# Optimization experiments

Hardware: AMD Instinct MI355X
Metric: run time of the kernel (lower is better)

## Reference

```python
import jax, jax.numpy as jnp
import numpy as np

N, K, D = 65536, 1024, 512


def setup_inputs() -> dict:
    key = jax.random.key(0)
    k1, k2, k3 = jax.random.split(key, 3)
    x = jax.random.normal(k1, (N, D), dtype=jnp.float32)
    y = jax.random.randint(k2, (N,), 0, K)  # true/assigned cluster labels
    centers = jax.random.normal(k3, (K, D), dtype=jnp.float32)  # nn.Parameter
    return {"x": x, "y": y, "centers": centers}


def reference(x, y, centers):
    # caldis: squared euclidean distance from every point to every center.
    # original expand+sub+square+sum without materializing [N, K, D]).
    x2 = jnp.sum(x * x, axis=1, keepdims=True)          # [N, 1]
    c2 = jnp.sum(centers * centers, axis=1)              # [K]
    distance = x2 - 2.0 * (x @ centers.T) + c2           # [N, K]

    # predict: torch.sort(distance)[1][:, 0] == index of the smallest distance
    ynew = jnp.argmin(distance, axis=1)                  # [N]

    # calwei + calloss: one-hot(y) * distance summed == gather distance[i, y[i]]
    loss = jnp.sum(jnp.take_along_axis(distance, y[:, None], axis=1))

    return loss, ynew
```

## Files before the change

### kernel.cpp

```cpp
#include <hip/hip_runtime.h>

#define NPTS 65536
#define KC   1024
#define DD   512

using bf16x8 = __attribute__((ext_vector_type(8))) __bf16;
using f32x4  = __attribute__((ext_vector_type(4))) float;

__device__ __forceinline__ void gld_lds16(const void* g, void* lds_base) {
  __builtin_amdgcn_global_load_lds(
      (const __attribute__((address_space(1))) unsigned int*)(uintptr_t)g,
      (__attribute__((address_space(3))) unsigned int*)(unsigned int)(uintptr_t)lds_base,
      16, 0, 0);
}

__device__ __forceinline__ uint2 pack4(const float4& v) {
  uint2 r;
  r.x = (__float_as_uint(v.x) >> 16) | (__float_as_uint(v.y) & 0xffff0000u);
  r.y = (__float_as_uint(v.z) >> 16) | (__float_as_uint(v.w) & 0xffff0000u);
  return r;
}


__global__ __launch_bounds__(256) void convert_x_loss(
    const float* __restrict__ x, const int* __restrict__ y,
    const float* __restrict__ centers, uint4* __restrict__ xb,
    float* __restrict__ partial) {
  const int w = threadIdx.x >> 6, l = threadIdx.x & 63;
  const int row = blockIdx.x * 4 + w;
  const float4* xr = (const float4*)(x + (size_t)row * DD);
  float4 a = xr[2 * l];
  float4 b = xr[2 * l + 1];
  uint2 pa = pack4(a), pb = pack4(b);
  xb[row * 64 + l] = make_uint4(pa.x, pa.y, pb.x, pb.y);
  const int yr = y[row];
  const float4* cr = (const float4*)(centers + (size_t)yr * DD);
  float4 ca = cr[2 * l];
  float4 cb = cr[2 * l + 1];
  float d0 = a.x - ca.x, d1 = a.y - ca.y, d2 = a.z - ca.z, d3 = a.w - ca.w;
  float d4 = b.x - cb.x, d5 = b.y - cb.y, d6 = b.z - cb.z, d7 = b.w - cb.w;
  float s = d0 * d0 + d1 * d1 + d2 * d2 + d3 * d3 +
            d4 * d4 + d5 * d5 + d6 * d6 + d7 * d7;
#pragma unroll
  for (int off = 32; off; off >>= 1) s += __shfl_down(s, off, 64);
  __shared__ float ps[4];
  if (l == 0) ps[w] = s;
  __syncthreads();
  if (threadIdx.x == 0) partial[blockIdx.x] = ps[0] + ps[1] + ps[2] + ps[3];
}

__global__ __launch_bounds__(256) void convert_c(
    const float* __restrict__ centers, uint4* __restrict__ cb,
    float* __restrict__ c2) {
  const int row = (blockIdx.x * 256 + threadIdx.x) >> 6;
  const int l = threadIdx.x & 63;
  const float4* cf4 = (const float4*)centers;
  float4 a = cf4[row * 128 + 2 * l];
  float4 b = cf4[row * 128 + 2 * l + 1];
  uint2 pa = pack4(a), pb = pack4(b);
  cb[row * 64 + l] = make_uint4(pa.x, pa.y, pb.x, pb.y);
  float s = a.x * a.x + a.y * a.y + a.z * a.z + a.w * a.w +
            b.x * b.x + b.y * b.y + b.z * b.z + b.w * b.w;
#pragma unroll
  for (int off = 32; off; off >>= 1) s += __shfl_down(s, off, 64);
  if (l == 0) c2[row] = s;
}

__global__ __launch_bounds__(256, 2) void gemm_argmin(
    const uint4* __restrict__ xb, const uint4* __restrict__ cb,
    const float* __restrict__ c2, float* __restrict__ ynew_out) {
  __shared__ uint4 As[1024];
  __shared__ uint4 Bs[2048];
  __shared__ float c2s[1024];

  const int t = threadIdx.x;
  const int w = t >> 6, l = t & 63;
  const int wm = w >> 1, wn = w & 1;
  const int q4 = l >> 4, m16 = l & 15;
  const int row0 = blockIdx.x * 128;

#pragma unroll
  for (int i = 0; i < 4; i++) c2s[t + 256 * i] = c2[t + 256 * i];

  const int r_l = l >> 3;
  const int o_l = (l & 7) ^ r_l;
  int aidx[4];
#pragma unroll
  for (int q = 0; q < 4; q++)
    aidx[q] = (row0 + (w * 4 + q) * 8 + r_l) * 64 + o_l;
  int bsrc[8];
#pragma unroll
  for (int q = 0; q < 8; q++)
    bsrc[q] = ((w * 8 + q) * 8 + r_l) * 64 + o_l;

  const int xr = m16 & 7;

  float best[16];
  int bi_[16];
#pragma unroll
  for (int i = 0; i < 16; i++) { best[i] = 3.4e38f; bi_[i] = 0; }

  for (int n0 = 0; n0 < KC; n0 += 256) {
    f32x4 acc[4][8];
#pragma unroll
    for (int i = 0; i < 4; i++)
#pragma unroll
      for (int j = 0; j < 8; j++) acc[i][j] = (f32x4){0.f, 0.f, 0.f, 0.f};

    const uint4* bbase = cb + n0 * 64;

    for (int ks = 0; ks < 8; ks++) {
      __syncthreads();
#pragma unroll
      for (int q = 0; q < 4; q++)
        gld_lds16(xb + aidx[q] + ks * 8, &As[(w * 4 + q) * 64]);
#pragma unroll
      for (int q = 0; q < 8; q++)
        gld_lds16(bbase + bsrc[q] + ks * 8, &Bs[(w * 8 + q) * 64]);
      __syncthreads();
#pragma unroll
      for (int kk = 0; kk < 2; kk++) {
        const int oct = kk * 4 + q4;
        bf16x8 af[4];
#pragma unroll
        for (int i = 0; i < 4; i++) {
          const int ra = wm * 64 + i * 16 + m16;
          af[i] = *(const bf16x8*)&As[ra * 8 + (oct ^ xr)];
        }
#pragma unroll
        for (int j = 0; j < 8; j++) {
          const int rb = wn * 128 + j * 16 + m16;
          bf16x8 bf = *(const bf16x8*)&Bs[rb * 8 + (oct ^ xr)];
#pragma unroll
          for (int i = 0; i < 4; i++)
            acc[i][j] = __builtin_amdgcn_mfma_f32_16x16x32_bf16(af[i], bf, acc[i][j], 0, 0, 0);
        }
      }
    }

#pragma unroll
    for (int j = 0; j < 8; j++) {
      const int n = n0 + wn * 128 + j * 16 + m16;
      const float cc = c2s[n];
#pragma unroll
      for (int i = 0; i < 4; i++)
#pragma unroll
        for (int r = 0; r < 4; r++) {
          float v = fmaf(-2.f, acc[i][j][r], cc);
          const int bi = i * 4 + r;
          if (v < best[bi]) { best[bi] = v; bi_[bi] = n; }
        }
    }
  }

#pragma unroll
  for (int bi = 0; bi < 16; bi++) {
    float v = best[bi];
    int idx = bi_[bi];
#pragma unroll
    for (int off = 8; off; off >>= 1) {
      float ov = __shfl_xor(v, off, 64);
      int oi = __shfl_xor(idx, off, 64);
      if (ov < v || (ov == v && oi < idx)) { v = ov; idx = oi; }
    }
    if (m16 == 0) {
      const int m = wm * 64 + (bi >> 2) * 16 + q4 * 4 + (bi & 3);
      ynew_out[row0 + m] = (float)idx;
    }
  }
}

__global__ __launch_bounds__(256) void loss_final(const float* __restrict__ partial,
                                                  float* __restrict__ out) {
  float s = 0.f;
#pragma unroll
  for (int j = 0; j < 64; j++) s += partial[threadIdx.x + 256 * j];
#pragma unroll
  for (int off = 32; off; off >>= 1) s += __shfl_down(s, off, 64);
  __shared__ float ps[4];
  if ((threadIdx.x & 63) == 0) ps[threadIdx.x >> 6] = s;
  __syncthreads();
  if (threadIdx.x == 0) out[0] = ps[0] + ps[1] + ps[2] + ps[3];
}


#define SLOT(row, oct) (16 * (oct) + (((row) & 15) ^ (((oct) & 2) << 1)))

__device__ __forceinline__ void split_pack(const float4& a, const float4& b,
                                           uint4& hi, uint4& lo) {
  float f[8] = {a.x, a.y, a.z, a.w, b.x, b.y, b.z, b.w};
  uint hw[4], lw[4];
#pragma unroll
  for (int i = 0; i < 4; i++) {
    uint e0 = __float_as_uint(f[2 * i]), e1 = __float_as_uint(f[2 * i + 1]);
    hw[i] = (e0 >> 16) | (e1 & 0xffff0000u);
    float l0 = f[2 * i]     - __uint_as_float(e0 & 0xffff0000u);
    float l1 = f[2 * i + 1] - __uint_as_float(e1 & 0xffff0000u);
    lw[i] = (__float_as_uint(l0) >> 16) | (__float_as_uint(l1) & 0xffff0000u);
  }
  hi = make_uint4(hw[0], hw[1], hw[2], hw[3]);
  lo = make_uint4(lw[0], lw[1], lw[2], lw[3]);
}

__global__ __launch_bounds__(256) void c2_kernel(const float* __restrict__ centers,
                                                 float* __restrict__ c2) {
  int wave = (blockIdx.x * 256 + threadIdx.x) >> 6;
  int lane = threadIdx.x & 63;
  const float4* c4 = (const float4*)(centers + (size_t)wave * DD);
  float s = 0.f;
#pragma unroll
  for (int j = 0; j < 2; j++) {
    float4 v = c4[lane + 64 * j];
    s += v.x * v.x + v.y * v.y + v.z * v.z + v.w * v.w;
  }
#pragma unroll
  for (int off = 32; off; off >>= 1) s += __shfl_down(s, off, 64);
  if (lane == 0) c2[wave] = s;
}

__global__ __launch_bounds__(256, 2) void argmin_fb(
    const float* __restrict__ x, const float* __restrict__ centers,
    const float* __restrict__ c2, float* __restrict__ ynew_out) {
  __shared__ uint4 Ah[512], Al[512], Bh[512], Bl[512];
  const int t = threadIdx.x;
  const int w = t >> 6, l = t & 63;
  const int wm = w >> 1, wn = w & 1;
  const size_t row0 = (size_t)blockIdx.x * 128;
  const int srow = t >> 1, h = t & 1;
  const int mt = srow >> 4;
  const int so0 = mt * 64 + SLOT(srow, 2 * h);
  const int so1 = mt * 64 + SLOT(srow, 2 * h + 1);
  const int rs = SLOT(l & 15, l >> 4);
  const float* xp = x + (row0 + srow) * DD + h * 16;
  float best[16];
  int bidx[16];
#pragma unroll
  for (int i = 0; i < 16; i++) { best[i] = 3.4e38f; bidx[i] = 0; }
  for (int n0 = 0; n0 < KC; n0 += 128) {
    const float* bp = centers + (size_t)(n0 + srow) * DD + h * 16;
    f32x4 acc[4][4];
#pragma unroll
    for (int i = 0; i < 4; i++)
#pragma unroll
      for (int j = 0; j < 4; j++) acc[i][j] = (f32x4){0.f, 0.f, 0.f, 0.f};
    float4 ra[4], rb[4];
#pragma unroll
    for (int q = 0; q < 4; q++) {
      ra[q] = *(const float4*)(xp + q * 4);
      rb[q] = *(const float4*)(bp + q * 4);
    }
    for (int ks = 0; ks < 16; ks++) {
      uint4 ah0, al0, ah1, al1, bh0, bl0, bh1, bl1;
      split_pack(ra[0], ra[1], ah0, al0);
      split_pack(ra[2], ra[3], ah1, al1);
      split_pack(rb[0], rb[1], bh0, bl0);
      split_pack(rb[2], rb[3], bh1, bl1);
      __syncthreads();
      Ah[so0] = ah0; Al[so0] = al0;
      Ah[so1] = ah1; Al[so1] = al1;
      Bh[so0] = bh0; Bl[so0] = bl0;
      Bh[so1] = bh1; Bl[so1] = bl1;
      __syncthreads();
      if (ks < 15) {
#pragma unroll
        for (int q = 0; q < 4; q++) {
          ra[q] = *(const float4*)(xp + (ks + 1) * 32 + q * 4);
          rb[q] = *(const float4*)(bp + (ks + 1) * 32 + q * 4);
        }
      }
      bf16x8 afh[4], afl[4], bfh[4], bfl[4];
#pragma unroll
      for (int i = 0; i < 4; i++) {
        afh[i] = *(const bf16x8*)&Ah[(wm * 4 + i) * 64 + rs];
        afl[i] = *(const bf16x8*)&Al[(wm * 4 + i) * 64 + rs];
        bfh[i] = *(const bf16x8*)&Bh[(wn * 4 + i) * 64 + rs];
        bfl[i] = *(const bf16x8*)&Bl[(wn * 4 + i) * 64 + rs];
      }
#pragma unroll
      for (int i = 0; i < 4; i++)
#pragma unroll
        for (int j = 0; j < 4; j++) {
          acc[i][j] = __builtin_amdgcn_mfma_f32_16x16x32_bf16(afh[i], bfh[j], acc[i][j], 0, 0, 0);
          acc[i][j] = __builtin_amdgcn_mfma_f32_16x16x32_bf16(afl[i], bfh[j], acc[i][j], 0, 0, 0);
          acc[i][j] = __builtin_amdgcn_mfma_f32_16x16x32_bf16(afh[i], bfl[j], acc[i][j], 0, 0, 0);
        }
    }
#pragma unroll
    for (int j = 0; j < 4; j++) {
      int n = n0 + wn * 64 + j * 16 + (l & 15);
      float cc = c2[n];
#pragma unroll
      for (int i = 0; i < 4; i++)
#pragma unroll
        for (int r = 0; r < 4; r++) {
          float v = fmaf(-2.f, acc[i][j][r], cc);
          int bi = i * 4 + r;
          if (v < best[bi]) { best[bi] = v; bidx[bi] = n; }
        }
    }
  }
#pragma unroll
  for (int bi = 0; bi < 16; bi++) {
    float v = best[bi];
    int idx = bidx[bi];
#pragma unroll
    for (int off = 8; off; off >>= 1) {
      float ov = __shfl_xor(v, off, 64);
      int oi = __shfl_xor(idx, off, 64);
      if (ov < v || (ov == v && oi < idx)) { v = ov; idx = oi; }
    }
    if ((l & 15) == 0) {
      int m = wm * 64 + (bi >> 2) * 16 + (l >> 4) * 4 + (bi & 3);
      ynew_out[row0 + m] = (float)idx;
    }
  }
}

__global__ __launch_bounds__(256) void loss_partial_fb(
    const float* __restrict__ x, const int* __restrict__ y,
    const float* __restrict__ centers, float* __restrict__ partial) {
  const int w = threadIdx.x >> 6, l = threadIdx.x & 63;
  const int row = blockIdx.x * 4 + w;
  const float4* x4 = (const float4*)(x + (size_t)row * DD);
  const float4* c4 = (const float4*)(centers + (size_t)y[row] * DD);
  float s = 0.f;
#pragma unroll
  for (int j = 0; j < 2; j++) {
    float4 xv = x4[2 * l + j], cv = c4[2 * l + j];
    float dx = xv.x - cv.x, dy = xv.y - cv.y, dz = xv.z - cv.z, dw = xv.w - cv.w;
    s += dx * dx + dy * dy + dz * dz + dw * dw;
  }
#pragma unroll
  for (int off = 32; off; off >>= 1) s += __shfl_down(s, off, 64);
  __shared__ float ps[4];
  if (l == 0) ps[w] = s;
  __syncthreads();
  if (threadIdx.x == 0) partial[blockIdx.x] = ps[0] + ps[1] + ps[2] + ps[3];
}


extern "C" void kernel_launch(void* const* d_in, const int* in_sizes, int n_in,
                              void* d_out, int out_size, void* d_ws, size_t ws_size,
                              hipStream_t stream) {
  const float* x       = (const float*)d_in[0];
  const int*   y       = (const int*)d_in[1];
  const float* centers = (const float*)d_in[2];
  float* out = (float*)d_out;

  const size_t xb_bytes = (size_t)NPTS * DD * 2;
  const size_t cb_bytes = (size_t)KC * DD * 2;
  const size_t need = xb_bytes + cb_bytes + (KC + NPTS / 4) * sizeof(float);

  if (ws_size >= need) {
    uint4* xb      = (uint4*)d_ws;
    uint4* cbp     = (uint4*)((char*)d_ws + xb_bytes);
    float* c2      = (float*)((char*)d_ws + xb_bytes + cb_bytes);
    float* partial = c2 + KC;
    convert_c<<<KC / 4, 256, 0, stream>>>(centers, cbp, c2);
    convert_x_loss<<<NPTS / 4, 256, 0, stream>>>(x, y, centers, xb, partial);
    gemm_argmin<<<NPTS / 128, 256, 0, stream>>>(xb, cbp, c2, out + 1);
    loss_final<<<1, 256, 0, stream>>>(partial, out);
  } else {
    float* c2      = (float*)d_ws;
    float* partial = c2 + KC;
    c2_kernel<<<KC / 4, 256, 0, stream>>>(centers, c2);
    argmin_fb<<<NPTS / 128, 256, 0, stream>>>(x, centers, c2, out + 1);
    loss_partial_fb<<<NPTS / 4, 256, 0, stream>>>(x, y, centers, partial);
    loss_final<<<1, 256, 0, stream>>>(partial, out);
  }
}
```

Before: 274.0 us.

## Compute loss via GEMM-side gather, merge prep kernels, raise occupancy hint

Instead of gathering centers[y] per row and computing the exact difference norm, the loss is now split into sum of ||x||^2 (accumulated in a merged prep kernel) plus the -2x·c+||c||^2 term picked up inside the GEMM epilogue when the column equals the row's label. The centers and x conversion kernels are merged into one launch, which drops a launch and the extra read of the gathered center rows. The GEMM launch bound goes from 2 to 3 blocks per CU. The loss now uses bf16 dot products, which may reduce accuracy, and the added compare may raise register pressure under the tighter occupancy bound.

```diff
diff --git a/kernel.cpp b/kernel.cpp
--- a/kernel.cpp
+++ b/kernel.cpp
@@ -22,56 +22,56 @@
 }
 
 
-__global__ __launch_bounds__(256) void convert_x_loss(
-    const float* __restrict__ x, const int* __restrict__ y,
-    const float* __restrict__ centers, uint4* __restrict__ xb,
-    float* __restrict__ partial) {
+__global__ __launch_bounds__(256) void prep_kernel(
+    const float* __restrict__ x, const float* __restrict__ centers,
+    uint4* __restrict__ xb, uint4* __restrict__ cb,
+    float* __restrict__ c2, float* __restrict__ px2) {
   const int w = threadIdx.x >> 6, l = threadIdx.x & 63;
-  const int row = blockIdx.x * 4 + w;
-  const float4* xr = (const float4*)(x + (size_t)row * DD);
-  float4 a = xr[2 * l];
-  float4 b = xr[2 * l + 1];
-  uint2 pa = pack4(a), pb = pack4(b);
-  xb[row * 64 + l] = make_uint4(pa.x, pa.y, pb.x, pb.y);
-  const int yr = y[row];
-  const float4* cr = (const float4*)(centers + (size_t)yr * DD);
-  float4 ca = cr[2 * l];
-  float4 cb = cr[2 * l + 1];
-  float d0 = a.x - ca.x, d1 = a.y - ca.y, d2 = a.z - ca.z, d3 = a.w - ca.w;
-  float d4 = b.x - cb.x, d5 = b.y - cb.y, d6 = b.z - cb.z, d7 = b.w - cb.w;
-  float s = d0 * d0 + d1 * d1 + d2 * d2 + d3 * d3 +
-            d4 * d4 + d5 * d5 + d6 * d6 + d7 * d7;
+  if (blockIdx.x < 256) {
+    const int row = blockIdx.x * 4 + w;
+    const float4* cf4 = (const float4*)centers;
+    float4 a = cf4[row * 128 + 2 * l];
+    float4 b = cf4[row * 128 + 2 * l + 1];
+    uint2 pa = pack4(a), pb = pack4(b);
+    cb[row * 64 + l] = make_uint4(pa.x, pa.y, pb.x, pb.y);
+    float s = a.x * a.x + a.y * a.y + a.z * a.z + a.w * a.w +
+              b.x * b.x + b.y * b.y + b.z * b.z + b.w * b.w;
+#pragma unroll
+    for (int off = 32; off; off >>= 1) s += __shfl_down(s, off, 64);
+    if (l == 0) c2[row] = s;
+    return;
+  }
+  const int xblk = blockIdx.x - 256;
+  const int base = xblk * 32 + w * 8;
+  const float4* xf4 = (const float4*)x;
+  float s = 0.f;
+#pragma unroll
+  for (int p = 0; p < 8; p++) {
+    const int row = base + p;
+    float4 a = xf4[row * 128 + 2 * l];
+    float4 b = xf4[row * 128 + 2 * l + 1];
+    uint2 pa = pack4(a), pb = pack4(b);
+    xb[row * 64 + l] = make_uint4(pa.x, pa.y, pb.x, pb.y);
+    s += a.x * a.x + a.y * a.y + a.z * a.z + a.w * a.w +
+         b.x * b.x + b.y * b.y + b.z * b.z + b.w * b.w;
+  }
 #pragma unroll
   for (int off = 32; off; off >>= 1) s += __shfl_down(s, off, 64);
   __shared__ float ps[4];
   if (l == 0) ps[w] = s;
   __syncthreads();
-  if (threadIdx.x == 0) partial[blockIdx.x] = ps[0] + ps[1] + ps[2] + ps[3];
-}
-
-__global__ __launch_bounds__(256) void convert_c(
-    const float* __restrict__ centers, uint4* __restrict__ cb,
-    float* __restrict__ c2) {
-  const int row = (blockIdx.x * 256 + threadIdx.x) >> 6;
-  const int l = threadIdx.x & 63;
-  const float4* cf4 = (const float4*)centers;
-  float4 a = cf4[row * 128 + 2 * l];
-  float4 b = cf4[row * 128 + 2 * l + 1];
-  uint2 pa = pack4(a), pb = pack4(b);
-  cb[row * 64 + l] = make_uint4(pa.x, pa.y, pb.x, pb.y);
-  float s = a.x * a.x + a.y * a.y + a.z * a.z + a.w * a.w +
-            b.x * b.x + b.y * b.y + b.z * b.z + b.w * b.w;
-#pragma unroll
-  for (int off = 32; off; off >>= 1) s += __shfl_down(s, off, 64);
-  if (l == 0) c2[row] = s;
-}
-
-__global__ __launch_bounds__(256, 2) void gemm_argmin(
+  if (threadIdx.x == 0) px2[xblk] = ps[0] + ps[1] + ps[2] + ps[3];
+}
+
+__global__ __launch_bounds__(256, 3) void gemm_argmin(
     const uint4* __restrict__ xb, const uint4* __restrict__ cb,
-    const float* __restrict__ c2, float* __restrict__ ynew_out) {
+    const float* __restrict__ c2, const int* __restrict__ y,
+    float* __restrict__ ynew_out, float* __restrict__ ploss) {
   __shared__ uint4 As[1024];
   __shared__ uint4 Bs[2048];
   __shared__ float c2s[1024];
+  __shared__ int   ys[128];
+  __shared__ float lred[4];
 
   const int t = threadIdx.x;
   const int w = t >> 6, l = t & 63;
@@ -81,6 +81,15 @@
 
 #pragma unroll
   for (int i = 0; i < 4; i++) c2s[t + 256 * i] = c2[t + 256 * i];
+  if (t < 128) ys[t] = y[row0 + t];
+  __syncthreads();
+
+  int ysv[16];
+#pragma unroll
+  for (int i = 0; i < 4; i++)
+#pragma unroll
+    for (int r = 0; r < 4; r++)
+      ysv[i * 4 + r] = ys[wm * 64 + i * 16 + q4 * 4 + r];
 
   const int r_l = l >> 3;
   const int o_l = (l & 7) ^ r_l;
@@ -99,6 +108,7 @@
   int bi_[16];
 #pragma unroll
   for (int i = 0; i < 16; i++) { best[i] = 3.4e38f; bi_[i] = 0; }
+  float lsum = 0.f;
 
   for (int n0 = 0; n0 < KC; n0 += 256) {
     f32x4 acc[4][8];
@@ -148,6 +158,7 @@
         for (int r = 0; r < 4; r++) {
           float v = fmaf(-2.f, acc[i][j][r], cc);
           const int bi = i * 4 + r;
+          if (n == ysv[bi]) lsum += v;
           if (v < best[bi]) { best[bi] = v; bi_[bi] = n; }
         }
     }
@@ -168,13 +179,22 @@
       ynew_out[row0 + m] = (float)idx;
     }
   }
-}
-
-__global__ __launch_bounds__(256) void loss_final(const float* __restrict__ partial,
+
+#pragma unroll
+  for (int off = 32; off; off >>= 1) lsum += __shfl_down(lsum, off, 64);
+  if (l == 0) lred[w] = lsum;
+  __syncthreads();
+  if (t == 0) ploss[blockIdx.x] = lred[0] + lred[1] + lred[2] + lred[3];
+}
+
+__global__ __launch_bounds__(256) void loss_final(const float* __restrict__ px2,
+                                                  const float* __restrict__ ploss,
                                                   float* __restrict__ out) {
   float s = 0.f;
 #pragma unroll
-  for (int j = 0; j < 64; j++) s += partial[threadIdx.x + 256 * j];
+  for (int j = 0; j < 8; j++) s += px2[threadIdx.x + 256 * j];
+#pragma unroll
+  for (int j = 0; j < 2; j++) s += ploss[threadIdx.x + 256 * j];
 #pragma unroll
   for (int off = 32; off; off >>= 1) s += __shfl_down(s, off, 64);
   __shared__ float ps[4];
@@ -338,6 +358,19 @@
   if (threadIdx.x == 0) partial[blockIdx.x] = ps[0] + ps[1] + ps[2] + ps[3];
 }
 
+__global__ __launch_bounds__(256) void loss_final_fb(const float* __restrict__ partial,
+                                                     float* __restrict__ out) {
+  float s = 0.f;
+#pragma unroll
+  for (int j = 0; j < 64; j++) s += partial[threadIdx.x + 256 * j];
+#pragma unroll
+  for (int off = 32; off; off >>= 1) s += __shfl_down(s, off, 64);
+  __shared__ float ps[4];
+  if ((threadIdx.x & 63) == 0) ps[threadIdx.x >> 6] = s;
+  __syncthreads();
+  if (threadIdx.x == 0) out[0] = ps[0] + ps[1] + ps[2] + ps[3];
+}
+
 
 extern "C" void kernel_launch(void* const* d_in, const int* in_sizes, int n_in,
                               void* d_out, int out_size, void* d_ws, size_t ws_size,
@@ -349,23 +382,23 @@
 
   const size_t xb_bytes = (size_t)NPTS * DD * 2;
   const size_t cb_bytes = (size_t)KC * DD * 2;
-  const size_t need = xb_bytes + cb_bytes + (KC + NPTS / 4) * sizeof(float);
+  const size_t need = xb_bytes + cb_bytes + (KC + 2048 + 512) * sizeof(float);
 
   if (ws_size >= need) {
-    uint4* xb      = (uint4*)d_ws;
-    uint4* cbp     = (uint4*)((char*)d_ws + xb_bytes);
-    float* c2      = (float*)((char*)d_ws + xb_bytes + cb_bytes);
-    float* partial = c2 + KC;
-    convert_c<<<KC / 4, 256, 0, stream>>>(centers, cbp, c2);
-    convert_x_loss<<<NPTS / 4, 256, 0, stream>>>(x, y, centers, xb, partial);
-    gemm_argmin<<<NPTS / 128, 256, 0, stream>>>(xb, cbp, c2, out + 1);
-    loss_final<<<1, 256, 0, stream>>>(partial, out);
+    uint4* xb    = (uint4*)d_ws;
+    uint4* cbp   = (uint4*)((char*)d_ws + xb_bytes);
+    float* c2    = (float*)((char*)d_ws + xb_bytes + cb_bytes);
+    float* px2   = c2 + KC;
+    float* ploss = px2 + 2048;
+    prep_kernel<<<256 + 2048, 256, 0, stream>>>(x, centers, xb, cbp, c2, px2);
+    gemm_argmin<<<NPTS / 128, 256, 0, stream>>>(xb, cbp, c2, y, out + 1, ploss);
+    loss_final<<<1, 256, 0, stream>>>(px2, ploss, out);
   } else {
     float* c2      = (float*)d_ws;
     float* partial = c2 + KC;
     c2_kernel<<<KC / 4, 256, 0, stream>>>(centers, c2);
     argmin_fb<<<NPTS / 128, 256, 0, stream>>>(x, centers, c2, out + 1);
     loss_partial_fb<<<NPTS / 4, 256, 0, stream>>>(x, y, centers, partial);
-    loss_final<<<1, 256, 0, stream>>>(partial, out);
-  }
-}
+    loss_final_fb<<<1, 256, 0, stream>>>(partial, out);
+  }
+}
```

Result: slower. 314.2 us (+14.7%).
